# Optimization experiments

Hardware: AMD Instinct MI355X
Metric: run time of the kernel (lower is better)

The kernel has to match this reference:

```python
import jax, jax.numpy as jnp
import numpy as np

B, N, D = 4, 2048, 256
ALPHA = 0.2  # LeakyReLU negative slope
NEG = -1e9


def setup_inputs() -> dict:
    key = jax.random.key(0)
    ks = jax.random.split(key, 16)
    f = lambda k, s: jax.random.normal(k, s, dtype=jnp.float32)
    sc = 0.02
    spk = jax.random.randint(ks[13], (B, N), 0, 2)
    intra_mask = (spk[:, :, None] == spk[:, None, :]).astype(jnp.int32)
    inter_mask = 1 - intra_mask
    return {
        'inp': f(ks[0], (B, N, D)),
        'emo_vector': f(ks[1], (B, N, D)),
        'event_csk_before': f(ks[2], (B, N, D)),
        'event_csk_after': f(ks[3], (B, N, D)),
        'emo_intra_csk': f(ks[4], (B, N, D)),
        'emo_inter_csk': f(ks[5], (B, N, D)),
        'int_intra_csk': f(ks[6], (B, N, D)),
        'int_inter_csk': f(ks[7], (B, N, D)),
        'W': f(ks[8], (D, D)) * sc,
        'a': f(ks[9], (2 * D,)) * sc,
        'csk_W': f(ks[10], (D, D)) * sc,
        'csk_b': jnp.zeros((D,), jnp.float32),
        'emo_lin_W': f(ks[11], (4, D, D)) * sc,  # order: weight, query, key, value
        'emo_lin_b': jnp.zeros((4, D), jnp.float32),
        'act_lin_W': f(ks[12], (4, D, D)) * sc,
        'act_lin_b': jnp.zeros((4, D), jnp.float32),
        'conv_len': jax.random.randint(ks[14], (B,), N // 2, N + 1),
        'intra_mask': intra_mask,
        'inter_mask': inter_mask,
    }


def _csk_measure(tv, hv, temo, icsk, ocsk, tim, tom, lin_W, lin_b, add_emo):
    # tv/temo: [B,1,D] target vectors; hv: [B,N,D]; tim/tom: [B,1,N] float masks
    wW, qW, kW, vW = lin_W
    wb, qb, kb, vb = lin_b
    q = (tv + temo if add_emo else tv) @ qW + qb            # [B,1,D]
    w_i = icsk @ wW + wb
    w_o = ocsk @ wW + wb
    k_base = hv @ kW + kb
    v_base = hv @ vW + vb
    k_i, v_i = k_base + w_i, v_base + w_i                   # [B,N,D]
    k_o, v_o = k_base + w_o, v_base + w_o
    inv = 1.0 / jnp.sqrt(jnp.float32(D))
    s_i = jnp.einsum('bqd,bnd->bqn', q, k_i) * inv * tim    # [B,1,N]
    s_o = jnp.einsum('bqd,bnd->bqn', q, k_o) * inv * tom
    m = tim + tom
    probs = jax.nn.softmax(jnp.where(m == 0, NEG, s_i + s_o), axis=-1)  # [B,1,N]
    p_i = (probs * tim).transpose(0, 2, 1)                  # [B,N,1]
    p_o = (probs * tom).transpose(0, 2, 1)
    target_enh = p_i * q + p_o * q                          # q broadcasts [B,1,D]->[B,N,D]
    csk_enh = p_i * v_i + p_o * v_o
    return target_enh + csk_enh, probs


def reference(inp, emo_vector, event_csk_before, event_csk_after,
              emo_intra_csk, emo_inter_csk, int_intra_csk, int_inter_csk,
              W, a, csk_W, csk_b, emo_lin_W, emo_lin_b, act_lin_W, act_lin_b,
              conv_len, intra_mask, inter_mask):
    im = intra_mask.astype(jnp.float32)
    om = inter_mask.astype(jnp.float32)
    h = inp @ W                                             # [B,N,D]
    evt = (event_csk_after @ csk_W + csk_b) + (event_csk_before @ csk_W + csk_b)
    # GAT scoring without materializing [B,N,N,2D]:
    # e[b,i,j] = leaky_relu(h[b,i].a1 + (h+evt)[b,j].a2)
    a1, a2 = a[:D], a[D:]
    s1 = h @ a1                                             # [B,N]
    s2 = (h + evt) @ a2                                     # [B,N]
    e_pair = jax.nn.leaky_relu(s1[:, :, None] + s2[:, None, :], ALPHA)  # [B,N,N]
    e = e_pair * im + e_pair * om
    adj = im + om
    attention = jax.nn.softmax(jnp.where(adj == 0, NEG, e), axis=-1)
    h_prime = jnp.einsum('bij,bjd->bid', attention, h)      # [B,N,D]
    # gather target (last utterance) per conversation
    b_idx = jnp.arange(inp.shape[0])
    t_idx = conv_len - 1
    tv = inp[b_idx, t_idx][:, None, :]                      # [B,1,D]
    temo = emo_vector[b_idx, t_idx][:, None, :]
    tim = im[b_idx, t_idx][:, None, :]                      # [B,1,N]
    tom = om[b_idx, t_idx][:, None, :]
    emo_conn, emo_probs = _csk_measure(tv, h_prime, temo, emo_intra_csk,
                                       emo_inter_csk, tim, tom,
                                       emo_lin_W, emo_lin_b, add_emo=True)
    int_conn, act_probs = _csk_measure(tv, h_prime, temo, int_intra_csk,
                                       int_inter_csk, tim, tom,
                                       act_lin_W, act_lin_b, add_emo=False)
    out = h_prime + inp + emo_conn + int_conn
    return jax.nn.relu(out), emo_probs, act_probs
```

## Files before the change

### kernel.cpp

```cpp
#include <hip/hip_runtime.h>
#include <math.h>


namespace {
constexpr int B = 4, N = 2048, D = 256;
constexpr float ALPHA = 0.2f;
constexpr float INVS  = 0.0625f;

constexpr size_t OFF_H     = 0;
constexpr size_t OFF_HP    = 2097152;
constexpr size_t OFF_UE    = 4194304;
constexpr size_t OFF_UA    = 6291456;
constexpr size_t OFF_PPOS  = 8388608;
constexpr size_t OFF_PNEG  = 10486784;
constexpr size_t OFF_S1    = 12584960;
constexpr size_t OFF_S2    = OFF_S1 + 8192;
constexpr size_t OFF_SV    = OFF_S2 + 8192;
constexpr size_t OFF_SIDX  = OFF_SV + 8192;
constexpr size_t OFF_WP    = OFF_SIDX + 8192;
constexpr size_t OFF_WN    = OFF_WP + 8192;
constexpr size_t OFF_ZP    = OFF_WN + 8192;
constexpr size_t OFF_ZN    = OFF_ZP + 8196;
constexpr size_t OFF_PARTP = OFF_ZN + 8196;
constexpr size_t OFF_PARTN = OFF_PARTP + 32768;
constexpr size_t OFF_LE    = OFF_PARTN + 32768;
constexpr size_t OFF_LA    = OFF_LE + 8192;
constexpr size_t OFF_SET   = OFF_LA + 8192;
constexpr size_t KQE = OFF_SET + 0;
constexpr size_t WQE = OFF_SET + 1024;
constexpr size_t KQA = OFF_SET + 2048;
constexpr size_t WQA = OFF_SET + 3072;
constexpr size_t QCE = OFF_SET + 4096;
constexpr size_t QCA = OFF_SET + 5120;
constexpr size_t CA2 = OFF_SET + 6144;
constexpr size_t CEc = OFF_SET + 6400;
constexpr size_t CAc = OFF_SET + 6404;
constexpr size_t C2c = OFF_SET + 6408;
constexpr size_t OFF_RNK   = OFF_SET + 8192;
constexpr size_t OFF_C0    = OFF_RNK + 8192;
constexpr size_t OFF_C1    = OFF_C0 + 8192;
constexpr size_t OFF_PARTQ = OFF_C1 + 8192;
constexpr size_t OFF_QE    = OFF_PARTQ + 32768;
constexpr size_t OFF_QA    = OFF_QE + 1024;
constexpr size_t OFF_BT    = OFF_QA + 1024;
constexpr size_t OFF_PCNT  = OFF_BT + 163840;
constexpr size_t OFF_LEU   = OFF_PCNT + 131072;
constexpr size_t OFF_LAU   = OFF_LEU + 8192;
constexpr size_t SMXE      = OFF_LAU + 8192;
constexpr size_t SIVE      = SMXE + 4;
constexpr size_t SMXA      = SIVE + 4;
constexpr size_t SIVA      = SMXA + 4;
}

typedef __attribute__((ext_vector_type(8))) short bf16x8;
typedef __attribute__((ext_vector_type(4))) float f32x4;

__device__ inline float wave_sum(float v) {
#pragma unroll
  for (int off = 32; off > 0; off >>= 1) v += __shfl_xor(v, off, 64);
  return v;
}

__device__ inline ushort f2bf(float x) {
  union { float f; uint u; } v; v.f = x;
  return (ushort)((v.u + 0x7FFFu + ((v.u >> 16) & 1u)) >> 16);
}
__device__ inline uint pk2bf(float a, float b) {
  return (uint)f2bf(a) | ((uint)f2bf(b) << 16);
}

__global__ __launch_bounds__(256) void k_btq(
    const float* __restrict__ Wm, const float* __restrict__ eW,
    const float* __restrict__ aW, const float* __restrict__ inp,
    const float* __restrict__ emo, const int* __restrict__ cl,
    ushort* __restrict__ bt, float* __restrict__ ws)
{
  __shared__ float smem[64*65];
  if (blockIdx.y < 5) {
    int m = blockIdx.y;
    const float* src = (m == 0) ? Wm : (m == 1) ? eW + 3*65536 : (m == 2) ? eW
                     : (m == 3) ? aW + 3*65536 : aW;
    ushort* dst = bt + (size_t)m*65536;
    int k0 = (blockIdx.x >> 2)*64, n0 = (blockIdx.x & 3)*64;
    int r = threadIdx.x >> 2, c0 = (threadIdx.x & 3)*16;
#pragma unroll
    for (int cc = 0; cc < 16; cc += 4)
      *(float4*)&smem[r*65 + c0+cc] = *(const float4*)&src[(size_t)(k0+r)*256 + n0 + c0 + cc];
    __syncthreads();
    int n = threadIdx.x >> 2, kq = (threadIdx.x & 3)*16;
    uint4 o0, o1;
    o0.x = pk2bf(smem[(kq+ 0)*65+n], smem[(kq+ 1)*65+n]);
    o0.y = pk2bf(smem[(kq+ 2)*65+n], smem[(kq+ 3)*65+n]);
    o0.z = pk2bf(smem[(kq+ 4)*65+n], smem[(kq+ 5)*65+n]);
    o0.w = pk2bf(smem[(kq+ 6)*65+n], smem[(kq+ 7)*65+n]);
    o1.x = pk2bf(smem[(kq+ 8)*65+n], smem[(kq+ 9)*65+n]);
    o1.y = pk2bf(smem[(kq+10)*65+n], smem[(kq+11)*65+n]);
    o1.z = pk2bf(smem[(kq+12)*65+n], smem[(kq+13)*65+n]);
    o1.w = pk2bf(smem[(kq+14)*65+n], smem[(kq+15)*65+n]);
    *(uint4*)&dst[(size_t)(n0+n)*256 + k0 + kq]     = o0;
    *(uint4*)&dst[(size_t)(n0+n)*256 + k0 + kq + 8] = o1;
  } else {
    int c = blockIdx.x;
    int m = blockIdx.y - 5;
    int d = threadIdx.x;
    if (d < 64) {
      int b = d >> 4, kk = d & 15;
      int t = cl[b] - 1;
      size_t idx = ((size_t)b*N + t)*D + c*16 + kk;
      float v = inp[idx];
      if (m == 0) v += emo[idx];
      smem[b*16 + kk] = v;
    }
    __syncthreads();
    const float* Wq = (m ? aW : eW) + (size_t)D*D;
    float acc0 = 0.f, acc1 = 0.f, acc2 = 0.f, acc3 = 0.f;
#pragma unroll
    for (int kk = 0; kk < 16; ++kk) {
      int k = c*16 + kk;
      float w = Wq[(size_t)k*D + d];
      acc0 += smem[0*16+kk]*w; acc1 += smem[1*16+kk]*w;
      acc2 += smem[2*16+kk]*w; acc3 += smem[3*16+kk]*w;
    }
    size_t base = OFF_PARTQ + ((size_t)(m*16 + c)*4)*256 + d;
    ws[base + 0*256] = acc0; ws[base + 1*256] = acc1;
    ws[base + 2*256] = acc2; ws[base + 3*256] = acc3;
  }
}

__global__ __launch_bounds__(256) void k_mgemmh(
    const float* __restrict__ A1, const ushort* __restrict__ bt,
    float* __restrict__ C)
{
  __shared__ ushort As[32*40];
  const int t = threadIdx.x;
  const int lane = t & 63, w = t >> 6;
  const int laneN = lane & 15, kg = lane >> 4;
  const int m0 = blockIdx.x * 32, n0 = blockIdx.y * 128;
  const int srow = t >> 3, sc = (t & 7) * 4;
  f32x4 acc[2][2] = {};
  for (int k0 = 0; k0 < 256; k0 += 32) {
    __syncthreads();
    float4 f = *(const float4*)&A1[(size_t)(m0 + srow)*256 + k0 + sc];
    uint2 o; o.x = pk2bf(f.x, f.y); o.y = pk2bf(f.z, f.w);
    *(uint2*)&As[srow*40 + sc] = o;
    __syncthreads();
    bf16x8 af[2];
#pragma unroll
    for (int i = 0; i < 2; ++i)
      af[i] = *(const bf16x8*)&As[(i*16 + laneN)*40 + kg*8];
#pragma unroll
    for (int j = 0; j < 2; ++j) {
      bf16x8 bf = *(const bf16x8*)&bt[(size_t)(n0 + w*32 + j*16 + laneN)*256 + k0 + kg*8];
#pragma unroll
      for (int i = 0; i < 2; ++i)
        acc[i][j] = __builtin_amdgcn_mfma_f32_16x16x32_bf16(af[i], bf, acc[i][j], 0, 0, 0);
    }
  }
#pragma unroll
  for (int i = 0; i < 2; ++i)
#pragma unroll
    for (int j = 0; j < 2; ++j)
#pragma unroll
      for (int r = 0; r < 4; ++r)
        C[(size_t)(m0 + i*16 + kg*4 + r)*256 + n0 + w*32 + j*16 + laneN] = acc[i][j][r];
}

__global__ __launch_bounds__(256) void k_qfinish(
    const float* __restrict__ eb, const float* __restrict__ ab,
    const float* __restrict__ cskb, const float* __restrict__ a,
    float* __restrict__ ws)
{
  int b = blockIdx.x, m = blockIdx.y, d = threadIdx.x;
  __shared__ float red[D];
  const float* bias = m ? ab : eb;
  float q = bias[D + d];
#pragma unroll
  for (int c = 0; c < 16; ++c)
    q += ws[OFF_PARTQ + ((size_t)(m*16 + c)*4 + b)*256 + d];
  ws[(m ? OFF_QA : OFF_QE) + (size_t)b*D + d] = q;
  ws[(m ? QCA : QCE) + (size_t)b*D + d] = q + bias[3*D + d] + bias[0*D + d];
  red[d] = q * (bias[2*D + d] + bias[0*D + d]);
  __syncthreads();
  for (int s = 128; s > 0; s >>= 1) { if (d < s) red[d] += red[d+s]; __syncthreads(); }
  if (d == 0) ws[(m ? CAc : CEc) + b] = red[0];
  if (m == 1 && b == 0) {
    __syncthreads();
    red[d] = cskb[d] * a[D + d];
    __syncthreads();
    for (int s = 128; s > 0; s >>= 1) { if (d < s) red[d] += red[d+s]; __syncthreads(); }
    if (d == 0) ws[C2c] = 2.0f * red[0];
  }
}

__global__ __launch_bounds__(256) void k_rowdots(
    const float* __restrict__ eW, const float* __restrict__ aW,
    const float* __restrict__ cskW, const float* __restrict__ a,
    float* __restrict__ ws)
{
  int job = blockIdx.y;
  int wid = threadIdx.x >> 6, lane = threadIdx.x & 63;
  int row = blockIdx.x*4 + wid;
  __shared__ float vec[D];
  const float* M; size_t outo;
  if (job < 16) {
    int b = job >> 2, m = (job >> 1) & 1, which = job & 1;
    const float* base = m ? aW : eW;
    M = base + (which ? 0 : (size_t)2*D*D);
    if (threadIdx.x < D)
      vec[threadIdx.x] = ws[(m ? OFF_QA : OFF_QE) + (size_t)b*D + threadIdx.x];
    outo = (which ? (m ? WQA : WQE) : (m ? KQA : KQE)) + (size_t)b*D;
  } else {
    M = cskW;
    if (threadIdx.x < D) vec[threadIdx.x] = a[D + threadIdx.x];
    outo = CA2;
  }
  __syncthreads();
  float4 w = *reinterpret_cast<const float4*>(&M[(size_t)row*D + lane*4]);
  float s = w.x*vec[lane*4] + w.y*vec[lane*4+1] + w.z*vec[lane*4+2] + w.w*vec[lane*4+3];
  s = wave_sum(s);
  if (lane == 0) ws[outo + row] = s;
}

__global__ __launch_bounds__(256) void k_u(
    const float* __restrict__ ei, const float* __restrict__ eo,
    const float* __restrict__ ai, const float* __restrict__ ao,
    const int* __restrict__ cl, const int* __restrict__ intra,
    float* __restrict__ ws)
{
  size_t g = (size_t)blockIdx.x*256 + threadIdx.x;
  size_t base = g << 2;
  int b = (int)(base >> 19);
  int n = (int)((base >> 8) & (N - 1));
  int d0 = (int)(base & (D - 1));
  int t = cl[b] - 1;
  float tm = (float)intra[(size_t)b*N*N + (size_t)t*N + n];
  float om = 1.0f - tm;
  float4 vei = *(const float4*)&ei[base];
  float4 veo = *(const float4*)&eo[base];
  float4 vai = *(const float4*)&ai[base];
  float4 vao = *(const float4*)&ao[base];
  float4 ue, ua;
  ue.x = tm*vei.x + om*veo.x; ue.y = tm*vei.y + om*veo.y;
  ue.z = tm*vei.z + om*veo.z; ue.w = tm*vei.w + om*veo.w;
  ua.x = tm*vai.x + om*vao.x; ua.y = tm*vai.y + om*vao.y;
  ua.z = tm*vai.z + om*vao.z; ua.w = tm*vai.w + om*vao.w;
  *(float4*)&ws[OFF_UE + base] = ue;
  *(float4*)&ws[OFF_UA + base] = ua;
  float4 wqe = *(const float4*)&ws[WQE + (size_t)b*D + d0];
  float4 wqa = *(const float4*)&ws[WQA + (size_t)b*D + d0];
  float se = ue.x*wqe.x + ue.y*wqe.y + ue.z*wqe.z + ue.w*wqe.w;
  float sa = ua.x*wqa.x + ua.y*wqa.y + ua.z*wqa.z + ua.w*wqa.w;
  se = wave_sum(se); sa = wave_sum(sa);
  if ((threadIdx.x & 63) == 0) {
    size_t row = base >> 8;
    ws[OFF_LEU + row] = se;
    ws[OFF_LAU + row] = sa;
  }
}

__global__ __launch_bounds__(256) void k_s12(
    const float* __restrict__ bef, const float* __restrict__ aft,
    const float* __restrict__ a, float* __restrict__ ws)
{
  int wid  = (int)(((size_t)blockIdx.x*256 + threadIdx.x) >> 6);
  int lane = threadIdx.x & 63;
  int d0 = lane << 2;
  float4 a1 = *(const float4*)&a[d0];
  float4 a2 = *(const float4*)&a[D + d0];
  float4 cv = *(const float4*)&ws[CA2 + d0];
  float c2  = ws[C2c];
  for (int rr = 0; rr < 4; ++rr) {
    int row = wid*4 + rr;
    float4 h4 = *(const float4*)&ws[OFF_H + (size_t)row*D + d0];
    float4 b4 = *(const float4*)&bef[(size_t)row*D + d0];
    float4 f4 = *(const float4*)&aft[(size_t)row*D + d0];
    float s1 = h4.x*a1.x + h4.y*a1.y + h4.z*a1.z + h4.w*a1.w;
    float s2 = h4.x*a2.x + h4.y*a2.y + h4.z*a2.z + h4.w*a2.w
             + (b4.x+f4.x)*cv.x + (b4.y+f4.y)*cv.y
             + (b4.z+f4.z)*cv.z + (b4.w+f4.w)*cv.w;
    s1 = wave_sum(s1); s2 = wave_sum(s2);
    if (lane == 0) { ws[OFF_S1 + row] = s1; ws[OFF_S2 + row] = s2 + c2; }
  }
}

__global__ __launch_bounds__(256) void k_cnt2(float* __restrict__ ws)
{
  int jb = blockIdx.x;
  int kb = blockIdx.y;
  int b  = blockIdx.z;
  int tid = threadIdx.x;
  __shared__ float ck[128];
  if (tid < 32)
    *(float4*)&ck[tid*4] = *(const float4*)&ws[OFF_S2 + (size_t)b*N + kb*128 + tid*4];
  __syncthreads();
  int j = jb*256 + tid;
  float v = ws[OFF_S2 + (size_t)b*N + j];
  int kg = kb*128;
  int cnt = 0;
#pragma unroll
  for (int k = 0; k < 128; k += 16) {
    float4 u0 = *(const float4*)&ck[k];
    float4 u1 = *(const float4*)&ck[k+4];
    float4 u2 = *(const float4*)&ck[k+8];
    float4 u3 = *(const float4*)&ck[k+12];
    cnt += (u0.x < v) || (u0.x == v && (kg+k+ 0) < j);
    cnt += (u0.y < v) || (u0.y == v && (kg+k+ 1) < j);
    cnt += (u0.z < v) || (u0.z == v && (kg+k+ 2) < j);
    cnt += (u0.w < v) || (u0.w == v && (kg+k+ 3) < j);
    cnt += (u1.x < v) || (u1.x == v && (kg+k+ 4) < j);
    cnt += (u1.y < v) || (u1.y == v && (kg+k+ 5) < j);
    cnt += (u1.z < v) || (u1.z == v && (kg+k+ 6) < j);
    cnt += (u1.w < v) || (u1.w == v && (kg+k+ 7) < j);
    cnt += (u2.x < v) || (u2.x == v && (kg+k+ 8) < j);
    cnt += (u2.y < v) || (u2.y == v && (kg+k+ 9) < j);
    cnt += (u2.z < v) || (u2.z == v && (kg+k+10) < j);
    cnt += (u2.w < v) || (u2.w == v && (kg+k+11) < j);
    cnt += (u3.x < v) || (u3.x == v && (kg+k+12) < j);
    cnt += (u3.y < v) || (u3.y == v && (kg+k+13) < j);
    cnt += (u3.z < v) || (u3.z == v && (kg+k+14) < j);
    cnt += (u3.w < v) || (u3.w == v && (kg+k+15) < j);
  }
  ((int*)ws)[OFF_PCNT + ((size_t)(b*16 + kb))*N + j] = cnt;
}

__global__ __launch_bounds__(256) void k_cntfin(float* __restrict__ ws)
{
  int b = blockIdx.y;
  int j = blockIdx.x*256 + threadIdx.x;
  int cnt = 0;
#pragma unroll
  for (int kb = 0; kb < 16; ++kb)
    cnt += ((const int*)ws)[OFF_PCNT + ((size_t)(b*16 + kb))*N + j];
  float v = ws[OFF_S2 + (size_t)b*N + j];
  size_t o = (size_t)b*N + cnt;
  ws[OFF_SV + o] = v;
  ((int*)ws)[OFF_SIDX + o] = j;
  ws[OFF_WP + o] = expf(v);
  ws[OFF_WN + o] = expf(ALPHA*v);
}

__global__ __launch_bounds__(1024) void k_scan(float* __restrict__ ws)
{
  int b = blockIdx.x, m = blockIdx.y, t = threadIdx.x;
  const float* src = ws + (m ? OFF_WN : OFF_WP) + (size_t)b*N;
  float* dst = ws + (m ? OFF_ZN : OFF_ZP) + (size_t)b*(N+1);
  __shared__ float buf[N];
  buf[t] = src[t]; buf[t + 1024] = src[t + 1024];
  __syncthreads();
  for (int off = 1; off < N; off <<= 1) {
    float v0 = (t >= off)        ? buf[t - off]        : 0.f;
    float v1 = (t + 1024 >= off) ? buf[t + 1024 - off] : 0.f;
    __syncthreads();
    buf[t] += v0; buf[t + 1024] += v1;
    __syncthreads();
  }
  if (t == 0) dst[0] = 0.f;
  dst[t + 1]    = buf[t];
  dst[t + 1025] = buf[t + 1024];
}

__global__ __launch_bounds__(256) void k_rank(float* __restrict__ ws)
{
  int b = blockIdx.y;
  int i = blockIdx.x * 256 + threadIdx.x;
  __shared__ float sv[N];
  for (int r = threadIdx.x; r < N; r += 256) sv[r] = ws[OFF_SV + (size_t)b*N + r];
  __syncthreads();
  float s1i = ws[OFF_S1 + (size_t)b*N + i];
  float th = -s1i;
  int lo = 0, hi = N;
  while (lo < hi) { int mid = (lo + hi) >> 1; if (sv[mid] <= th) lo = mid + 1; else hi = mid; }
  int r = lo;
  float ep = expf(s1i), en = expf(ALPHA*s1i);
  float zp  = ws[OFF_ZP + (size_t)b*(N+1) + r];
  float zn  = ws[OFF_ZN + (size_t)b*(N+1) + r];
  float zpT = ws[OFF_ZP + (size_t)b*(N+1) + N];
  float den = ep*(zpT - zp) + en*zn;
  ((int*)ws)[OFF_RNK + (size_t)b*N + i] = r;
  ws[OFF_C0 + (size_t)b*N + i] = ep/den;
  ws[OFF_C1 + (size_t)b*N + i] = en/den;
}

__global__ __launch_bounds__(256) void k_p1(float* __restrict__ ws)
{
  int c = blockIdx.x, b = blockIdx.y, d = threadIdx.x;
  const int*   sidx = (const int*)ws + OFF_SIDX + (size_t)b*N;
  const float* wp = ws + OFF_WP + (size_t)b*N;
  const float* wn = ws + OFF_WN + (size_t)b*N;
  const float* h  = ws + OFF_H + (size_t)b*N*D;
  float ap = 0.f, an = 0.f;
  for (int r = c*64; r < c*64 + 64; ++r) {
    float hv = h[(size_t)sidx[r]*D + d];
    ap += wp[r]*hv; an += wn[r]*hv;
  }
  ws[OFF_PARTP + ((size_t)b*32 + c)*D + d] = ap;
  ws[OFF_PARTN + ((size_t)b*32 + c)*D + d] = an;
}

__global__ __launch_bounds__(256) void k_p3(float* __restrict__ ws)
{
  int c = blockIdx.x, b = blockIdx.y, d = threadIdx.x;
  const int*   sidx = (const int*)ws + OFF_SIDX + (size_t)b*N;
  const float* wp = ws + OFF_WP + (size_t)b*N;
  const float* wn = ws + OFF_WN + (size_t)b*N;
  const float* h  = ws + OFF_H + (size_t)b*N*D;
  float ap = 0.f, an = 0.f;
  for (int c2 = 0; c2 < c; ++c2) {
    ap += ws[OFF_PARTP + ((size_t)b*32 + c2)*D + d];
    an += ws[OFF_PARTN + ((size_t)b*32 + c2)*D + d];
  }
  for (int r = c*64; r < c*64 + 64; ++r) {
    ws[OFF_PPOS + ((size_t)b*(N+1) + r)*D + d] = ap;
    ws[OFF_PNEG + ((size_t)b*(N+1) + r)*D + d] = an;
    float hv = h[(size_t)sidx[r]*D + d];
    ap += wp[r]*hv; an += wn[r]*hv;
  }
  if (c == 31) {
    ws[OFF_PPOS + ((size_t)b*(N+1) + N)*D + d] = ap;
    ws[OFF_PNEG + ((size_t)b*(N+1) + N)*D + d] = an;
  }
}

__global__ __launch_bounds__(256) void k_hprime2(float* __restrict__ ws)
{
  int b = blockIdx.y, d = threadIdx.x;
  int i0 = blockIdx.x * 8;
  float totp = ws[OFF_PPOS + ((size_t)b*(N+1) + N)*D + d];
  float kqe = ws[KQE + (size_t)b*D + d];
  float kqa = ws[KQA + (size_t)b*D + d];
  float se[8], sa[8];
#pragma unroll
  for (int ii = 0; ii < 8; ++ii) {
    int i = i0 + ii;
    int   r  = ((const int*)ws)[OFF_RNK + (size_t)b*N + i];
    float c0 = ws[OFF_C0 + (size_t)b*N + i];
    float c1 = ws[OFF_C1 + (size_t)b*N + i];
    float pp = ws[OFF_PPOS + ((size_t)b*(N+1) + r)*D + d];
    float pn = ws[OFF_PNEG + ((size_t)b*(N+1) + r)*D + d];
    float v = c0*(totp - pp) + c1*pn;
    ws[OFF_HP + ((size_t)b*N + i)*D + d] = v;
    se[ii] = v*kqe;
    sa[ii] = v*kqa;
  }
  __shared__ float lred[16][4];
  int w = d >> 6, lane = d & 63;
#pragma unroll
  for (int ii = 0; ii < 8; ++ii) {
    float s = wave_sum(se[ii]);
    if (lane == 0) lred[ii][w] = s;
    s = wave_sum(sa[ii]);
    if (lane == 0) lred[8 + ii][w] = s;
  }
  __syncthreads();
  if (d < 16) {
    float s = lred[d][0] + lred[d][1] + lred[d][2] + lred[d][3];
    size_t row = (size_t)b*N + i0 + (d & 7);
    if (d < 8) ws[OFF_LE + row] = (s + ws[OFF_LEU + row] + ws[CEc + b]) * INVS;
    else       ws[OFF_LA + row] = (s + ws[OFF_LAU + row] + ws[CAc + b]) * INVS;
  }
}

__global__ __launch_bounds__(256) void k_smred(float* __restrict__ ws)
{
  int b = blockIdx.x, m = blockIdx.y, t = threadIdx.x;
  const float* l = ws + (m ? OFF_LA : OFF_LE) + (size_t)b*N;
  __shared__ float red[256];
  float v[8];
  float mx = -1e30f;
#pragma unroll
  for (int k = 0; k < 8; ++k) { v[k] = l[t*8 + k]; mx = fmaxf(mx, v[k]); }
  red[t] = mx; __syncthreads();
  for (int s = 128; s > 0; s >>= 1) { if (t < s) red[t] = fmaxf(red[t], red[t+s]); __syncthreads(); }
  mx = red[0]; __syncthreads();
  float sum = 0.f;
#pragma unroll
  for (int k = 0; k < 8; ++k) sum += expf(v[k] - mx);
  red[t] = sum; __syncthreads();
  for (int s = 128; s > 0; s >>= 1) { if (t < s) red[t] += red[t+s]; __syncthreads(); }
  if (t == 0) {
    ws[(m ? SMXA : SMXE) + b] = mx;
    ws[(m ? SIVA : SIVE) + b] = 1.0f / red[0];
  }
}

__global__ __launch_bounds__(256) void k_tail(
    const float* __restrict__ inp, const ushort* __restrict__ bt,
    float* __restrict__ ws, float* __restrict__ out)
{
  __shared__ ushort Hs[32*40], Es[32*40], Zs[32*40];
  __shared__ float qec[256], qac[256];
  const int t = threadIdx.x;
  const int m0 = blockIdx.x * 32, n0 = blockIdx.y * 128;
  const int b = m0 >> 11;
  const int lane = t & 63, w = t >> 6;
  const int laneN = lane & 15, kg = lane >> 4;
  qec[t] = ws[QCE + (size_t)b*D + t];
  qac[t] = ws[QCA + (size_t)b*D + t];
  const int srow = t >> 3, sc = (t & 7) * 4;
  const float* hp = ws + OFF_HP;
  const float* ue = ws + OFF_UE;
  const float* ua = ws + OFF_UA;
  const ushort* Bve = bt + 1*65536;
  const ushort* Bwe = bt + 2*65536;
  const ushort* Bva = bt + 3*65536;
  const ushort* Bwa = bt + 4*65536;
  f32x4 accE[2][2] = {}, accA[2][2] = {};
  for (int k0 = 0; k0 < 256; k0 += 32) {
    __syncthreads();
    size_t abase = (size_t)(m0 + srow)*256 + k0 + sc;
    float4 h4 = *(const float4*)&hp[abase];
    float4 e4 = *(const float4*)&ue[abase];
    float4 z4 = *(const float4*)&ua[abase];
    uint2 oh; oh.x = pk2bf(h4.x, h4.y); oh.y = pk2bf(h4.z, h4.w);
    uint2 oe; oe.x = pk2bf(e4.x, e4.y); oe.y = pk2bf(e4.z, e4.w);
    uint2 oz; oz.x = pk2bf(z4.x, z4.y); oz.y = pk2bf(z4.z, z4.w);
    *(uint2*)&Hs[srow*40 + sc] = oh;
    *(uint2*)&Es[srow*40 + sc] = oe;
    *(uint2*)&Zs[srow*40 + sc] = oz;
    __syncthreads();
    bf16x8 hf[2], ef[2], zf[2];
#pragma unroll
    for (int i = 0; i < 2; ++i) {
      hf[i] = *(const bf16x8*)&Hs[(i*16 + laneN)*40 + kg*8];
      ef[i] = *(const bf16x8*)&Es[(i*16 + laneN)*40 + kg*8];
      zf[i] = *(const bf16x8*)&Zs[(i*16 + laneN)*40 + kg*8];
    }
#pragma unroll
    for (int j = 0; j < 2; ++j) {
      size_t cb = (size_t)(n0 + w*32 + j*16 + laneN)*256 + k0 + kg*8;
      bf16x8 bve = *(const bf16x8*)&Bve[cb];
      bf16x8 bwe = *(const bf16x8*)&Bwe[cb];
      bf16x8 bva = *(const bf16x8*)&Bva[cb];
      bf16x8 bwa = *(const bf16x8*)&Bwa[cb];
#pragma unroll
      for (int i = 0; i < 2; ++i) {
        accE[i][j] = __builtin_amdgcn_mfma_f32_16x16x32_bf16(hf[i], bve, accE[i][j], 0, 0, 0);
        accE[i][j] = __builtin_amdgcn_mfma_f32_16x16x32_bf16(ef[i], bwe, accE[i][j], 0, 0, 0);
        accA[i][j] = __builtin_amdgcn_mfma_f32_16x16x32_bf16(hf[i], bva, accA[i][j], 0, 0, 0);
        accA[i][j] = __builtin_amdgcn_mfma_f32_16x16x32_bf16(zf[i], bwa, accA[i][j], 0, 0, 0);
      }
    }
  }
  float smxe = ws[SMXE + b], sive = ws[SIVE + b];
  float smxa = ws[SMXA + b], siva = ws[SIVA + b];
  if (blockIdx.y == 0 && t < 32) {
    size_t row = (size_t)m0 + t;
    int n = (int)(row & (N - 1));
    float pe = expf(ws[OFF_LE + row] - smxe) * sive;
    float pa = expf(ws[OFF_LA + row] - smxa) * siva;
    out[(size_t)B*N*D + (size_t)b*N + n] = pe;
    out[(size_t)B*N*D + (size_t)B*N + (size_t)b*N + n] = pa;
  }
#pragma unroll
  for (int i = 0; i < 2; ++i) {
#pragma unroll
    for (int r = 0; r < 4; ++r) {
      size_t row = (size_t)m0 + i*16 + kg*4 + r;
      float pe = expf(ws[OFF_LE + row] - smxe) * sive;
      float pa = expf(ws[OFF_LA + row] - smxa) * siva;
#pragma unroll
      for (int j = 0; j < 2; ++j) {
        int col = n0 + w*32 + j*16 + laneN;
        size_t idx = row*256 + col;
        float o = hp[idx] + inp[idx] + pe*(qec[col] + accE[i][j][r]) + pa*(qac[col] + accA[i][j][r]);
        out[idx] = fmaxf(o, 0.f);
      }
    }
  }
}

extern "C" void kernel_launch(void* const* d_in, const int* in_sizes, int n_in,
                              void* d_out, int out_size, void* d_ws, size_t ws_size,
                              hipStream_t stream) {
  const float* inp  = (const float*)d_in[0];
  const float* emo  = (const float*)d_in[1];
  const float* bef  = (const float*)d_in[2];
  const float* aft  = (const float*)d_in[3];
  const float* ei   = (const float*)d_in[4];
  const float* eo   = (const float*)d_in[5];
  const float* ii   = (const float*)d_in[6];
  const float* io   = (const float*)d_in[7];
  const float* W    = (const float*)d_in[8];
  const float* a    = (const float*)d_in[9];
  const float* cskW = (const float*)d_in[10];
  const float* cskb = (const float*)d_in[11];
  const float* eW   = (const float*)d_in[12];
  const float* eb   = (const float*)d_in[13];
  const float* aW   = (const float*)d_in[14];
  const float* ab   = (const float*)d_in[15];
  const int*   cl   = (const int*)d_in[16];
  const int*   intra= (const int*)d_in[17];
  float* ws  = (float*)d_ws;
  float* out = (float*)d_out;
  ushort* bt = (ushort*)(ws + OFF_BT);

  k_btq<<<dim3(16, 7), 256, 0, stream>>>(W, eW, aW, inp, emo, cl, bt, ws);
  k_mgemmh<<<dim3(256, 2), 256, 0, stream>>>(inp, bt, ws + OFF_H);
  k_qfinish<<<dim3(B, 2), 256, 0, stream>>>(eb, ab, cskb, a, ws);
  k_rowdots<<<dim3(64, 17), 256, 0, stream>>>(eW, aW, cskW, a, ws);
  k_u<<<2048, 256, 0, stream>>>(ei, eo, ii, io, cl, intra, ws);
  k_s12<<<512, 256, 0, stream>>>(bef, aft, a, ws);
  k_cnt2<<<dim3(8, 16, B), 256, 0, stream>>>(ws);
  k_cntfin<<<dim3(8, B), 256, 0, stream>>>(ws);
  k_scan<<<dim3(B, 2), 1024, 0, stream>>>(ws);
  k_rank<<<dim3(8, B), 256, 0, stream>>>(ws);
  k_p1<<<dim3(32, B), 256, 0, stream>>>(ws);
  k_p3<<<dim3(32, B), 256, 0, stream>>>(ws);
  k_hprime2<<<dim3(256, B), 256, 0, stream>>>(ws);
  k_smred<<<dim3(B, 2), 256, 0, stream>>>(ws);
  k_tail<<<dim3(256, 2), 256, 0, stream>>>(inp, bt, ws, out);
}
```

Before: 123.3 us.

## Fuse nine tail kernels into one persistent kernel with grid-wide barriers

Replaces the nine separate launches (count, count-finish, scan, rank, p1, p3, hprime, softmax reduce, tail GEMM) with one 512-block persistent kernel whose phases are separated by a software grid barrier built on agent-scope atomics. The barrier counter is reset inside k_s12. The intent is to remove per-launch overhead and inter-kernel gaps across these small, latency-bound phases. The scan is also changed from a 1024-thread Hillis-Steele scan to per-thread serial sums of 8 elements followed by a 256-wide scan. Correctness depends on all 512 blocks being co-resident (launch bounds 256,2), and many phases leave most blocks idle while they spin at the barrier.

```diff
diff --git a/kernel.cpp b/kernel.cpp
--- a/kernel.cpp
+++ b/kernel.cpp
@@ -6,6 +6,7 @@
 constexpr int B = 4, N = 2048, D = 256;
 constexpr float ALPHA = 0.2f;
 constexpr float INVS  = 0.0625f;
+constexpr int NBLK = 512;
 
 constexpr size_t OFF_H     = 0;
 constexpr size_t OFF_HP    = 2097152;
@@ -50,6 +51,7 @@
 constexpr size_t SIVE      = SMXE + 4;
 constexpr size_t SMXA      = SIVE + 4;
 constexpr size_t SIVA      = SMXA + 4;
+constexpr size_t BARX      = SIVA + 4;
 }
 
 typedef __attribute__((ext_vector_type(8))) short bf16x8;
@@ -67,6 +69,26 @@
 }
 __device__ inline uint pk2bf(float a, float b) {
   return (uint)f2bf(a) | ((uint)f2bf(b) << 16);
+}
+
+__device__ inline void gbar(int* bar) {
+  __syncthreads();
+  if (threadIdx.x == 0) {
+    int* cnt = bar;
+    int* gen = bar + 1;
+    int g = __hip_atomic_load(gen, __ATOMIC_RELAXED, __HIP_MEMORY_SCOPE_AGENT);
+    __builtin_amdgcn_fence(__ATOMIC_RELEASE, "agent");
+    int a = __hip_atomic_fetch_add(cnt, 1, __ATOMIC_ACQ_REL, __HIP_MEMORY_SCOPE_AGENT);
+    if (a == NBLK - 1) {
+      __hip_atomic_store(cnt, 0, __ATOMIC_RELAXED, __HIP_MEMORY_SCOPE_AGENT);
+      __hip_atomic_store(gen, g + 1, __ATOMIC_RELEASE, __HIP_MEMORY_SCOPE_AGENT);
+    } else {
+      while (__hip_atomic_load(gen, __ATOMIC_RELAXED, __HIP_MEMORY_SCOPE_AGENT) == g)
+        __builtin_amdgcn_s_sleep(2);
+    }
+    __builtin_amdgcn_fence(__ATOMIC_ACQUIRE, "agent");
+  }
+  __syncthreads();
 }
 
 __global__ __launch_bounds__(256) void k_btq(
@@ -262,6 +284,10 @@
     const float* __restrict__ bef, const float* __restrict__ aft,
     const float* __restrict__ a, float* __restrict__ ws)
 {
+  if (blockIdx.x == 0 && threadIdx.x == 0) {
+    ((int*)ws)[BARX]     = 0;
+    ((int*)ws)[BARX + 1] = 0;
+  }
   int wid  = (int)(((size_t)blockIdx.x*256 + threadIdx.x) >> 6);
   int lane = threadIdx.x & 63;
   int d0 = lane << 2;
@@ -283,287 +309,299 @@
   }
 }
 
-__global__ __launch_bounds__(256) void k_cnt2(float* __restrict__ ws)
-{
-  int jb = blockIdx.x;
-  int kb = blockIdx.y;
-  int b  = blockIdx.z;
-  int tid = threadIdx.x;
-  __shared__ float ck[128];
-  if (tid < 32)
-    *(float4*)&ck[tid*4] = *(const float4*)&ws[OFF_S2 + (size_t)b*N + kb*128 + tid*4];
-  __syncthreads();
-  int j = jb*256 + tid;
-  float v = ws[OFF_S2 + (size_t)b*N + j];
-  int kg = kb*128;
-  int cnt = 0;
-#pragma unroll
-  for (int k = 0; k < 128; k += 16) {
-    float4 u0 = *(const float4*)&ck[k];
-    float4 u1 = *(const float4*)&ck[k+4];
-    float4 u2 = *(const float4*)&ck[k+8];
-    float4 u3 = *(const float4*)&ck[k+12];
-    cnt += (u0.x < v) || (u0.x == v && (kg+k+ 0) < j);
-    cnt += (u0.y < v) || (u0.y == v && (kg+k+ 1) < j);
-    cnt += (u0.z < v) || (u0.z == v && (kg+k+ 2) < j);
-    cnt += (u0.w < v) || (u0.w == v && (kg+k+ 3) < j);
-    cnt += (u1.x < v) || (u1.x == v && (kg+k+ 4) < j);
-    cnt += (u1.y < v) || (u1.y == v && (kg+k+ 5) < j);
-    cnt += (u1.z < v) || (u1.z == v && (kg+k+ 6) < j);
-    cnt += (u1.w < v) || (u1.w == v && (kg+k+ 7) < j);
-    cnt += (u2.x < v) || (u2.x == v && (kg+k+ 8) < j);
-    cnt += (u2.y < v) || (u2.y == v && (kg+k+ 9) < j);
-    cnt += (u2.z < v) || (u2.z == v && (kg+k+10) < j);
-    cnt += (u2.w < v) || (u2.w == v && (kg+k+11) < j);
-    cnt += (u3.x < v) || (u3.x == v && (kg+k+12) < j);
-    cnt += (u3.y < v) || (u3.y == v && (kg+k+13) < j);
-    cnt += (u3.z < v) || (u3.z == v && (kg+k+14) < j);
-    cnt += (u3.w < v) || (u3.w == v && (kg+k+15) < j);
-  }
-  ((int*)ws)[OFF_PCNT + ((size_t)(b*16 + kb))*N + j] = cnt;
-}
-
-__global__ __launch_bounds__(256) void k_cntfin(float* __restrict__ ws)
-{
-  int b = blockIdx.y;
-  int j = blockIdx.x*256 + threadIdx.x;
-  int cnt = 0;
-#pragma unroll
-  for (int kb = 0; kb < 16; ++kb)
-    cnt += ((const int*)ws)[OFF_PCNT + ((size_t)(b*16 + kb))*N + j];
-  float v = ws[OFF_S2 + (size_t)b*N + j];
-  size_t o = (size_t)b*N + cnt;
-  ws[OFF_SV + o] = v;
-  ((int*)ws)[OFF_SIDX + o] = j;
-  ws[OFF_WP + o] = expf(v);
-  ws[OFF_WN + o] = expf(ALPHA*v);
-}
-
-__global__ __launch_bounds__(1024) void k_scan(float* __restrict__ ws)
-{
-  int b = blockIdx.x, m = blockIdx.y, t = threadIdx.x;
-  const float* src = ws + (m ? OFF_WN : OFF_WP) + (size_t)b*N;
-  float* dst = ws + (m ? OFF_ZN : OFF_ZP) + (size_t)b*(N+1);
-  __shared__ float buf[N];
-  buf[t] = src[t]; buf[t + 1024] = src[t + 1024];
-  __syncthreads();
-  for (int off = 1; off < N; off <<= 1) {
-    float v0 = (t >= off)        ? buf[t - off]        : 0.f;
-    float v1 = (t + 1024 >= off) ? buf[t + 1024 - off] : 0.f;
-    __syncthreads();
-    buf[t] += v0; buf[t + 1024] += v1;
-    __syncthreads();
-  }
-  if (t == 0) dst[0] = 0.f;
-  dst[t + 1]    = buf[t];
-  dst[t + 1025] = buf[t + 1024];
-}
-
-__global__ __launch_bounds__(256) void k_rank(float* __restrict__ ws)
-{
-  int b = blockIdx.y;
-  int i = blockIdx.x * 256 + threadIdx.x;
-  __shared__ float sv[N];
-  for (int r = threadIdx.x; r < N; r += 256) sv[r] = ws[OFF_SV + (size_t)b*N + r];
-  __syncthreads();
-  float s1i = ws[OFF_S1 + (size_t)b*N + i];
-  float th = -s1i;
-  int lo = 0, hi = N;
-  while (lo < hi) { int mid = (lo + hi) >> 1; if (sv[mid] <= th) lo = mid + 1; else hi = mid; }
-  int r = lo;
-  float ep = expf(s1i), en = expf(ALPHA*s1i);
-  float zp  = ws[OFF_ZP + (size_t)b*(N+1) + r];
-  float zn  = ws[OFF_ZN + (size_t)b*(N+1) + r];
-  float zpT = ws[OFF_ZP + (size_t)b*(N+1) + N];
-  float den = ep*(zpT - zp) + en*zn;
-  ((int*)ws)[OFF_RNK + (size_t)b*N + i] = r;
-  ws[OFF_C0 + (size_t)b*N + i] = ep/den;
-  ws[OFF_C1 + (size_t)b*N + i] = en/den;
-}
-
-__global__ __launch_bounds__(256) void k_p1(float* __restrict__ ws)
-{
-  int c = blockIdx.x, b = blockIdx.y, d = threadIdx.x;
-  const int*   sidx = (const int*)ws + OFF_SIDX + (size_t)b*N;
-  const float* wp = ws + OFF_WP + (size_t)b*N;
-  const float* wn = ws + OFF_WN + (size_t)b*N;
-  const float* h  = ws + OFF_H + (size_t)b*N*D;
-  float ap = 0.f, an = 0.f;
-  for (int r = c*64; r < c*64 + 64; ++r) {
-    float hv = h[(size_t)sidx[r]*D + d];
-    ap += wp[r]*hv; an += wn[r]*hv;
-  }
-  ws[OFF_PARTP + ((size_t)b*32 + c)*D + d] = ap;
-  ws[OFF_PARTN + ((size_t)b*32 + c)*D + d] = an;
-}
-
-__global__ __launch_bounds__(256) void k_p3(float* __restrict__ ws)
-{
-  int c = blockIdx.x, b = blockIdx.y, d = threadIdx.x;
-  const int*   sidx = (const int*)ws + OFF_SIDX + (size_t)b*N;
-  const float* wp = ws + OFF_WP + (size_t)b*N;
-  const float* wn = ws + OFF_WN + (size_t)b*N;
-  const float* h  = ws + OFF_H + (size_t)b*N*D;
-  float ap = 0.f, an = 0.f;
-  for (int c2 = 0; c2 < c; ++c2) {
-    ap += ws[OFF_PARTP + ((size_t)b*32 + c2)*D + d];
-    an += ws[OFF_PARTN + ((size_t)b*32 + c2)*D + d];
-  }
-  for (int r = c*64; r < c*64 + 64; ++r) {
-    ws[OFF_PPOS + ((size_t)b*(N+1) + r)*D + d] = ap;
-    ws[OFF_PNEG + ((size_t)b*(N+1) + r)*D + d] = an;
-    float hv = h[(size_t)sidx[r]*D + d];
-    ap += wp[r]*hv; an += wn[r]*hv;
-  }
-  if (c == 31) {
-    ws[OFF_PPOS + ((size_t)b*(N+1) + N)*D + d] = ap;
-    ws[OFF_PNEG + ((size_t)b*(N+1) + N)*D + d] = an;
-  }
-}
-
-__global__ __launch_bounds__(256) void k_hprime2(float* __restrict__ ws)
-{
-  int b = blockIdx.y, d = threadIdx.x;
-  int i0 = blockIdx.x * 8;
-  float totp = ws[OFF_PPOS + ((size_t)b*(N+1) + N)*D + d];
-  float kqe = ws[KQE + (size_t)b*D + d];
-  float kqa = ws[KQA + (size_t)b*D + d];
-  float se[8], sa[8];
-#pragma unroll
-  for (int ii = 0; ii < 8; ++ii) {
-    int i = i0 + ii;
-    int   r  = ((const int*)ws)[OFF_RNK + (size_t)b*N + i];
-    float c0 = ws[OFF_C0 + (size_t)b*N + i];
-    float c1 = ws[OFF_C1 + (size_t)b*N + i];
-    float pp = ws[OFF_PPOS + ((size_t)b*(N+1) + r)*D + d];
-    float pn = ws[OFF_PNEG + ((size_t)b*(N+1) + r)*D + d];
-    float v = c0*(totp - pp) + c1*pn;
-    ws[OFF_HP + ((size_t)b*N + i)*D + d] = v;
-    se[ii] = v*kqe;
-    sa[ii] = v*kqa;
-  }
-  __shared__ float lred[16][4];
-  int w = d >> 6, lane = d & 63;
-#pragma unroll
-  for (int ii = 0; ii < 8; ++ii) {
-    float s = wave_sum(se[ii]);
-    if (lane == 0) lred[ii][w] = s;
-    s = wave_sum(sa[ii]);
-    if (lane == 0) lred[8 + ii][w] = s;
-  }
-  __syncthreads();
-  if (d < 16) {
-    float s = lred[d][0] + lred[d][1] + lred[d][2] + lred[d][3];
-    size_t row = (size_t)b*N + i0 + (d & 7);
-    if (d < 8) ws[OFF_LE + row] = (s + ws[OFF_LEU + row] + ws[CEc + b]) * INVS;
-    else       ws[OFF_LA + row] = (s + ws[OFF_LAU + row] + ws[CAc + b]) * INVS;
-  }
-}
-
-__global__ __launch_bounds__(256) void k_smred(float* __restrict__ ws)
-{
-  int b = blockIdx.x, m = blockIdx.y, t = threadIdx.x;
-  const float* l = ws + (m ? OFF_LA : OFF_LE) + (size_t)b*N;
-  __shared__ float red[256];
-  float v[8];
-  float mx = -1e30f;
-#pragma unroll
-  for (int k = 0; k < 8; ++k) { v[k] = l[t*8 + k]; mx = fmaxf(mx, v[k]); }
-  red[t] = mx; __syncthreads();
-  for (int s = 128; s > 0; s >>= 1) { if (t < s) red[t] = fmaxf(red[t], red[t+s]); __syncthreads(); }
-  mx = red[0]; __syncthreads();
-  float sum = 0.f;
-#pragma unroll
-  for (int k = 0; k < 8; ++k) sum += expf(v[k] - mx);
-  red[t] = sum; __syncthreads();
-  for (int s = 128; s > 0; s >>= 1) { if (t < s) red[t] += red[t+s]; __syncthreads(); }
-  if (t == 0) {
-    ws[(m ? SMXA : SMXE) + b] = mx;
-    ws[(m ? SIVA : SIVE) + b] = 1.0f / red[0];
-  }
-}
-
-__global__ __launch_bounds__(256) void k_tail(
+__global__ __launch_bounds__(256, 2) void k_mega(
     const float* __restrict__ inp, const ushort* __restrict__ bt,
     float* __restrict__ ws, float* __restrict__ out)
 {
-  __shared__ ushort Hs[32*40], Es[32*40], Zs[32*40];
-  __shared__ float qec[256], qac[256];
+  __shared__ float smem[2304];
+  int* bar = (int*)ws + BARX;
+  const int gid = blockIdx.x;
   const int t = threadIdx.x;
-  const int m0 = blockIdx.x * 32, n0 = blockIdx.y * 128;
-  const int b = m0 >> 11;
-  const int lane = t & 63, w = t >> 6;
-  const int laneN = lane & 15, kg = lane >> 4;
-  qec[t] = ws[QCE + (size_t)b*D + t];
-  qac[t] = ws[QCA + (size_t)b*D + t];
-  const int srow = t >> 3, sc = (t & 7) * 4;
-  const float* hp = ws + OFF_HP;
-  const float* ue = ws + OFF_UE;
-  const float* ua = ws + OFF_UA;
-  const ushort* Bve = bt + 1*65536;
-  const ushort* Bwe = bt + 2*65536;
-  const ushort* Bva = bt + 3*65536;
-  const ushort* Bwa = bt + 4*65536;
-  f32x4 accE[2][2] = {}, accA[2][2] = {};
-  for (int k0 = 0; k0 < 256; k0 += 32) {
-    __syncthreads();
-    size_t abase = (size_t)(m0 + srow)*256 + k0 + sc;
-    float4 h4 = *(const float4*)&hp[abase];
-    float4 e4 = *(const float4*)&ue[abase];
-    float4 z4 = *(const float4*)&ua[abase];
-    uint2 oh; oh.x = pk2bf(h4.x, h4.y); oh.y = pk2bf(h4.z, h4.w);
-    uint2 oe; oe.x = pk2bf(e4.x, e4.y); oe.y = pk2bf(e4.z, e4.w);
-    uint2 oz; oz.x = pk2bf(z4.x, z4.y); oz.y = pk2bf(z4.z, z4.w);
-    *(uint2*)&Hs[srow*40 + sc] = oh;
-    *(uint2*)&Es[srow*40 + sc] = oe;
-    *(uint2*)&Zs[srow*40 + sc] = oz;
-    __syncthreads();
-    bf16x8 hf[2], ef[2], zf[2];
-#pragma unroll
-    for (int i = 0; i < 2; ++i) {
-      hf[i] = *(const bf16x8*)&Hs[(i*16 + laneN)*40 + kg*8];
-      ef[i] = *(const bf16x8*)&Es[(i*16 + laneN)*40 + kg*8];
-      zf[i] = *(const bf16x8*)&Zs[(i*16 + laneN)*40 + kg*8];
-    }
-#pragma unroll
-    for (int j = 0; j < 2; ++j) {
-      size_t cb = (size_t)(n0 + w*32 + j*16 + laneN)*256 + k0 + kg*8;
-      bf16x8 bve = *(const bf16x8*)&Bve[cb];
-      bf16x8 bwe = *(const bf16x8*)&Bwe[cb];
-      bf16x8 bva = *(const bf16x8*)&Bva[cb];
-      bf16x8 bwa = *(const bf16x8*)&Bwa[cb];
+
+  {
+    int jb = gid & 7, kb = (gid >> 3) & 15, b = gid >> 7;
+    float* ck = smem;
+    if (t < 32)
+      *(float4*)&ck[t*4] = *(const float4*)&ws[OFF_S2 + (size_t)b*N + kb*128 + t*4];
+    __syncthreads();
+    int j = jb*256 + t;
+    float v = ws[OFF_S2 + (size_t)b*N + j];
+    int kg = kb*128;
+    int cnt = 0;
+#pragma unroll
+    for (int k = 0; k < 128; k += 16) {
+      float4 u0 = *(const float4*)&ck[k];
+      float4 u1 = *(const float4*)&ck[k+4];
+      float4 u2 = *(const float4*)&ck[k+8];
+      float4 u3 = *(const float4*)&ck[k+12];
+      cnt += (u0.x < v) || (u0.x == v && (kg+k+ 0) < j);
+      cnt += (u0.y < v) || (u0.y == v && (kg+k+ 1) < j);
+      cnt += (u0.z < v) || (u0.z == v && (kg+k+ 2) < j);
+      cnt += (u0.w < v) || (u0.w == v && (kg+k+ 3) < j);
+      cnt += (u1.x < v) || (u1.x == v && (kg+k+ 4) < j);
+      cnt += (u1.y < v) || (u1.y == v && (kg+k+ 5) < j);
+      cnt += (u1.z < v) || (u1.z == v && (kg+k+ 6) < j);
+      cnt += (u1.w < v) || (u1.w == v && (kg+k+ 7) < j);
+      cnt += (u2.x < v) || (u2.x == v && (kg+k+ 8) < j);
+      cnt += (u2.y < v) || (u2.y == v && (kg+k+ 9) < j);
+      cnt += (u2.z < v) || (u2.z == v && (kg+k+10) < j);
+      cnt += (u2.w < v) || (u2.w == v && (kg+k+11) < j);
+      cnt += (u3.x < v) || (u3.x == v && (kg+k+12) < j);
+      cnt += (u3.y < v) || (u3.y == v && (kg+k+13) < j);
+      cnt += (u3.z < v) || (u3.z == v && (kg+k+14) < j);
+      cnt += (u3.w < v) || (u3.w == v && (kg+k+15) < j);
+    }
+    ((int*)ws)[OFF_PCNT + ((size_t)(b*16 + kb))*N + j] = cnt;
+  }
+  gbar(bar);
+
+  {
+    int tg = gid*256 + t;
+    if (tg < 8192) {
+      int b = tg >> 11, j = tg & (N - 1);
+      int cnt = 0;
+#pragma unroll
+      for (int kb = 0; kb < 16; ++kb)
+        cnt += ((const int*)ws)[OFF_PCNT + ((size_t)(b*16 + kb))*N + j];
+      float v = ws[OFF_S2 + (size_t)b*N + j];
+      size_t o = (size_t)b*N + cnt;
+      ws[OFF_SV + o] = v;
+      ((int*)ws)[OFF_SIDX + o] = j;
+      ws[OFF_WP + o] = expf(v);
+      ws[OFF_WN + o] = expf(ALPHA*v);
+    }
+  }
+  gbar(bar);
+
+  if (gid < 8) {
+    int b = gid >> 1, m = gid & 1;
+    const float* src = ws + (m ? OFF_WN : OFF_WP) + (size_t)b*N;
+    float* dst = ws + (m ? OFF_ZN : OFF_ZP) + (size_t)b*(N+1);
+    float* part = smem;
+    float vloc[8];
+    float s = 0.f;
+#pragma unroll
+    for (int k = 0; k < 8; ++k) { vloc[k] = src[t*8 + k]; s += vloc[k]; }
+    part[t] = s;
+    __syncthreads();
+    for (int off = 1; off < 256; off <<= 1) {
+      float v = (t >= off) ? part[t - off] : 0.f;
+      __syncthreads();
+      part[t] += v;
+      __syncthreads();
+    }
+    float run = (t == 0) ? 0.f : part[t-1];
+    if (t == 0) dst[0] = 0.f;
+#pragma unroll
+    for (int k = 0; k < 8; ++k) { run += vloc[k]; dst[t*8 + k + 1] = run; }
+  }
+  gbar(bar);
+
+  if (gid < 32) {
+    int b = gid >> 3;
+    for (int r = t; r < N; r += 256) smem[r] = ws[OFF_SV + (size_t)b*N + r];
+    __syncthreads();
+    int i = (gid & 7)*256 + t;
+    float s1i = ws[OFF_S1 + (size_t)b*N + i];
+    float th = -s1i;
+    int lo = 0, hi = N;
+    while (lo < hi) { int mid = (lo + hi) >> 1; if (smem[mid] <= th) lo = mid + 1; else hi = mid; }
+    float ep = expf(s1i), en = expf(ALPHA*s1i);
+    float zp  = ws[OFF_ZP + (size_t)b*(N+1) + lo];
+    float zn  = ws[OFF_ZN + (size_t)b*(N+1) + lo];
+    float zpT = ws[OFF_ZP + (size_t)b*(N+1) + N];
+    float den = ep*(zpT - zp) + en*zn;
+    ((int*)ws)[OFF_RNK + (size_t)b*N + i] = lo;
+    ws[OFF_C0 + (size_t)b*N + i] = ep/den;
+    ws[OFF_C1 + (size_t)b*N + i] = en/den;
+  }
+  gbar(bar);
+
+  if (gid < 128) {
+    int c = gid & 31, b = gid >> 5, d = t;
+    const int*   sidx = (const int*)ws + OFF_SIDX + (size_t)b*N;
+    const float* wp = ws + OFF_WP + (size_t)b*N;
+    const float* wn = ws + OFF_WN + (size_t)b*N;
+    const float* h  = ws + OFF_H + (size_t)b*N*D;
+    float ap = 0.f, an = 0.f;
+    for (int r = c*64; r < c*64 + 64; ++r) {
+      float hv = h[(size_t)sidx[r]*D + d];
+      ap += wp[r]*hv; an += wn[r]*hv;
+    }
+    ws[OFF_PARTP + ((size_t)b*32 + c)*D + d] = ap;
+    ws[OFF_PARTN + ((size_t)b*32 + c)*D + d] = an;
+  }
+  gbar(bar);
+
+  if (gid < 128) {
+    int c = gid & 31, b = gid >> 5, d = t;
+    const int*   sidx = (const int*)ws + OFF_SIDX + (size_t)b*N;
+    const float* wp = ws + OFF_WP + (size_t)b*N;
+    const float* wn = ws + OFF_WN + (size_t)b*N;
+    const float* h  = ws + OFF_H + (size_t)b*N*D;
+    float ap = 0.f, an = 0.f;
+    for (int c2 = 0; c2 < c; ++c2) {
+      ap += ws[OFF_PARTP + ((size_t)b*32 + c2)*D + d];
+      an += ws[OFF_PARTN + ((size_t)b*32 + c2)*D + d];
+    }
+    for (int r = c*64; r < c*64 + 64; ++r) {
+      ws[OFF_PPOS + ((size_t)b*(N+1) + r)*D + d] = ap;
+      ws[OFF_PNEG + ((size_t)b*(N+1) + r)*D + d] = an;
+      float hv = h[(size_t)sidx[r]*D + d];
+      ap += wp[r]*hv; an += wn[r]*hv;
+    }
+    if (c == 31) {
+      ws[OFF_PPOS + ((size_t)b*(N+1) + N)*D + d] = ap;
+      ws[OFF_PNEG + ((size_t)b*(N+1) + N)*D + d] = an;
+    }
+  }
+  gbar(bar);
+
+  {
+    float* lred = smem;
+    for (int sub = 0; sub < 2; ++sub) {
+      int task = gid*2 + sub;
+      int b = task >> 8;
+      int i0 = (task & 255)*8;
+      int d = t;
+      float totp = ws[OFF_PPOS + ((size_t)b*(N+1) + N)*D + d];
+      float kqe = ws[KQE + (size_t)b*D + d];
+      float kqa = ws[KQA + (size_t)b*D + d];
+      float se[8], sa[8];
+#pragma unroll
+      for (int ii = 0; ii < 8; ++ii) {
+        int i = i0 + ii;
+        int   r  = ((const int*)ws)[OFF_RNK + (size_t)b*N + i];
+        float c0 = ws[OFF_C0 + (size_t)b*N + i];
+        float c1 = ws[OFF_C1 + (size_t)b*N + i];
+        float pp = ws[OFF_PPOS + ((size_t)b*(N+1) + r)*D + d];
+        float pn = ws[OFF_PNEG + ((size_t)b*(N+1) + r)*D + d];
+        float v = c0*(totp - pp) + c1*pn;
+        ws[OFF_HP + ((size_t)b*N + i)*D + d] = v;
+        se[ii] = v*kqe;
+        sa[ii] = v*kqa;
+      }
+      int w = d >> 6, lane = d & 63;
+#pragma unroll
+      for (int ii = 0; ii < 8; ++ii) {
+        float s = wave_sum(se[ii]);
+        if (lane == 0) lred[ii*4 + w] = s;
+        s = wave_sum(sa[ii]);
+        if (lane == 0) lred[(8 + ii)*4 + w] = s;
+      }
+      __syncthreads();
+      if (d < 16) {
+        float s = lred[d*4+0] + lred[d*4+1] + lred[d*4+2] + lred[d*4+3];
+        size_t row = (size_t)b*N + i0 + (d & 7);
+        if (d < 8) ws[OFF_LE + row] = (s + ws[OFF_LEU + row] + ws[CEc + b]) * INVS;
+        else       ws[OFF_LA + row] = (s + ws[OFF_LAU + row] + ws[CAc + b]) * INVS;
+      }
+      __syncthreads();
+    }
+  }
+  gbar(bar);
+
+  if (gid < 8) {
+    int b = gid >> 1, m = gid & 1;
+    const float* l = ws + (m ? OFF_LA : OFF_LE) + (size_t)b*N;
+    float* red = smem;
+    float v[8];
+    float mx = -1e30f;
+#pragma unroll
+    for (int k = 0; k < 8; ++k) { v[k] = l[t*8 + k]; mx = fmaxf(mx, v[k]); }
+    red[t] = mx; __syncthreads();
+    for (int s = 128; s > 0; s >>= 1) { if (t < s) red[t] = fmaxf(red[t], red[t+s]); __syncthreads(); }
+    mx = red[0]; __syncthreads();
+    float sum = 0.f;
+#pragma unroll
+    for (int k = 0; k < 8; ++k) sum += expf(v[k] - mx);
+    red[t] = sum; __syncthreads();
+    for (int s = 128; s > 0; s >>= 1) { if (t < s) red[t] += red[t+s]; __syncthreads(); }
+    if (t == 0) {
+      ws[(m ? SMXA : SMXE) + b] = mx;
+      ws[(m ? SIVA : SIVE) + b] = 1.0f / red[0];
+    }
+  }
+  gbar(bar);
+
+  {
+    int bx = gid >> 1, by = gid & 1;
+    const int m0 = bx * 32, n0 = by * 128;
+    const int b = m0 >> 11;
+    const int lane = t & 63, w = t >> 6;
+    const int laneN = lane & 15, kg = lane >> 4;
+    float* qec = smem;
+    float* qac = smem + 256;
+    ushort* Hs = (ushort*)(smem + 512);
+    qec[t] = ws[QCE + (size_t)b*D + t];
+    qac[t] = ws[QCA + (size_t)b*D + t];
+    const int srow = t >> 3, sc = (t & 7) * 4;
+    const float* hp = ws + OFF_HP;
+    const ushort* Bve = bt + 1*65536;
+    const ushort* Bwe = bt + 2*65536;
+    const ushort* Bva = bt + 3*65536;
+    const ushort* Bwa = bt + 4*65536;
+    f32x4 accE[2][2] = {}, accA[2][2] = {};
+    for (int k0 = 0; k0 < 256; k0 += 32) {
+      __syncthreads();
+      size_t abase = (size_t)(m0 + srow)*256 + k0 + sc;
+      float4 h4 = *(const float4*)&hp[abase];
+      float4 e4 = *(const float4*)&ws[OFF_UE + abase];
+      float4 z4 = *(const float4*)&ws[OFF_UA + abase];
+      uint2 oh; oh.x = pk2bf(h4.x, h4.y); oh.y = pk2bf(h4.z, h4.w);
+      uint2 oe; oe.x = pk2bf(e4.x, e4.y); oe.y = pk2bf(e4.z, e4.w);
+      uint2 oz; oz.x = pk2bf(z4.x, z4.y); oz.y = pk2bf(z4.z, z4.w);
+      *(uint2*)&Hs[(srow)*40 + sc]            = oh;
+      *(uint2*)&Hs[(32 + srow)*40 + sc]       = oe;
+      *(uint2*)&Hs[(64 + srow)*40 + sc]       = oz;
+      __syncthreads();
+      bf16x8 hf[2], ef[2], zf[2];
 #pragma unroll
       for (int i = 0; i < 2; ++i) {
-        accE[i][j] = __builtin_amdgcn_mfma_f32_16x16x32_bf16(hf[i], bve, accE[i][j], 0, 0, 0);
-        accE[i][j] = __builtin_amdgcn_mfma_f32_16x16x32_bf16(ef[i], bwe, accE[i][j], 0, 0, 0);
-        accA[i][j] = __builtin_amdgcn_mfma_f32_16x16x32_bf16(hf[i], bva, accA[i][j], 0, 0, 0);
-        accA[i][j] = __builtin_amdgcn_mfma_f32_16x16x32_bf16(zf[i], bwa, accA[i][j], 0, 0, 0);
+        hf[i] = *(const bf16x8*)&Hs[(i*16 + laneN)*40 + kg*8];
+        ef[i] = *(const bf16x8*)&Hs[(32 + i*16 + laneN)*40 + kg*8];
+        zf[i] = *(const bf16x8*)&Hs[(64 + i*16 + laneN)*40 + kg*8];
       }
-    }
-  }
-  float smxe = ws[SMXE + b], sive = ws[SIVE + b];
-  float smxa = ws[SMXA + b], siva = ws[SIVA + b];
-  if (blockIdx.y == 0 && t < 32) {
-    size_t row = (size_t)m0 + t;
-    int n = (int)(row & (N - 1));
-    float pe = expf(ws[OFF_LE + row] - smxe) * sive;
-    float pa = expf(ws[OFF_LA + row] - smxa) * siva;
-    out[(size_t)B*N*D + (size_t)b*N + n] = pe;
-    out[(size_t)B*N*D + (size_t)B*N + (size_t)b*N + n] = pa;
-  }
-#pragma unroll
-  for (int i = 0; i < 2; ++i) {
-#pragma unroll
-    for (int r = 0; r < 4; ++r) {
-      size_t row = (size_t)m0 + i*16 + kg*4 + r;
+#pragma unroll
+      for (int j = 0; j < 2; ++j) {
+        size_t cb = (size_t)(n0 + w*32 + j*16 + laneN)*256 + k0 + kg*8;
+        bf16x8 bve = *(const bf16x8*)&Bve[cb];
+        bf16x8 bwe = *(const bf16x8*)&Bwe[cb];
+        bf16x8 bva = *(const bf16x8*)&Bva[cb];
+        bf16x8 bwa = *(const bf16x8*)&Bwa[cb];
+#pragma unroll
+        for (int i = 0; i < 2; ++i) {
+          accE[i][j] = __builtin_amdgcn_mfma_f32_16x16x32_bf16(hf[i], bve, accE[i][j], 0, 0, 0);
+          accE[i][j] = __builtin_amdgcn_mfma_f32_16x16x32_bf16(ef[i], bwe, accE[i][j], 0, 0, 0);
+          accA[i][j] = __builtin_amdgcn_mfma_f32_16x16x32_bf16(hf[i], bva, accA[i][j], 0, 0, 0);
+          accA[i][j] = __builtin_amdgcn_mfma_f32_16x16x32_bf16(zf[i], bwa, accA[i][j], 0, 0, 0);
+        }
+      }
+    }
+    float smxe = ws[SMXE + b], sive = ws[SIVE + b];
+    float smxa = ws[SMXA + b], siva = ws[SIVA + b];
+    if (by == 0 && t < 32) {
+      size_t row = (size_t)m0 + t;
+      int n = (int)(row & (N - 1));
       float pe = expf(ws[OFF_LE + row] - smxe) * sive;
       float pa = expf(ws[OFF_LA + row] - smxa) * siva;
-#pragma unroll
-      for (int j = 0; j < 2; ++j) {
-        int col = n0 + w*32 + j*16 + laneN;
-        size_t idx = row*256 + col;
-        float o = hp[idx] + inp[idx] + pe*(qec[col] + accE[i][j][r]) + pa*(qac[col] + accA[i][j][r]);
-        out[idx] = fmaxf(o, 0.f);
+      out[(size_t)B*N*D + (size_t)b*N + n] = pe;
+      out[(size_t)B*N*D + (size_t)B*N + (size_t)b*N + n] = pa;
+    }
+#pragma unroll
+    for (int i = 0; i < 2; ++i) {
+#pragma unroll
+      for (int r = 0; r < 4; ++r) {
+        size_t row = (size_t)m0 + i*16 + kg*4 + r;
+        float pe = expf(ws[OFF_LE + row] - smxe) * sive;
+        float pa = expf(ws[OFF_LA + row] - smxa) * siva;
+#pragma unroll
+        for (int j = 0; j < 2; ++j) {
+          int col = n0 + w*32 + j*16 + laneN;
+          size_t idx = row*256 + col;
+          float o = hp[idx] + inp[idx] + pe*(qec[col] + accE[i][j][r]) + pa*(qac[col] + accA[i][j][r]);
+          out[idx] = fmaxf(o, 0.f);
+        }
       }
     }
   }
@@ -600,13 +638,5 @@
   k_rowdots<<<dim3(64, 17), 256, 0, stream>>>(eW, aW, cskW, a, ws);
   k_u<<<2048, 256, 0, stream>>>(ei, eo, ii, io, cl, intra, ws);
   k_s12<<<512, 256, 0, stream>>>(bef, aft, a, ws);
-  k_cnt2<<<dim3(8, 16, B), 256, 0, stream>>>(ws);
-  k_cntfin<<<dim3(8, B), 256, 0, stream>>>(ws);
-  k_scan<<<dim3(B, 2), 1024, 0, stream>>>(ws);
-  k_rank<<<dim3(8, B), 256, 0, stream>>>(ws);
-  k_p1<<<dim3(32, B), 256, 0, stream>>>(ws);
-  k_p3<<<dim3(32, B), 256, 0, stream>>>(ws);
-  k_hprime2<<<dim3(256, B), 256, 0, stream>>>(ws);
-  k_smred<<<dim3(B, 2), 256, 0, stream>>>(ws);
-  k_tail<<<dim3(256, 2), 256, 0, stream>>>(inp, bt, ws, out);
-}
+  k_mega<<<NBLK, 256, 0, stream>>>(inp, bt, ws, out);
+}
```

After: 370.8 us. +200.8%, slower.
